# Kernel optimization log

Hardware: AMD Instinct MI355X
Metric: run time of the kernel (lower is better)

## Reference

```python
import jax, jax.numpy as jnp
import numpy as np

LN_EPS = 1e-5
BOUNDARY_ID = 0  # boundary_ids = {space_id} = {0}


def setup_inputs() -> dict:
    key = jax.random.key(0)
    k1, k2, k3 = jax.random.split(key, 3)
    B, T, D = 16, 8192, 256
    x = jax.random.normal(k1, (B, T, D), dtype=jnp.float32)
    input_ids = jax.random.randint(k2, (B, T), 0, 8, dtype=jnp.int64)
    W_proj = jax.random.normal(k3, (D, D), dtype=jnp.float32) / np.sqrt(D)
    b_proj = jnp.zeros((D,), dtype=jnp.float32)
    gamma = jnp.ones((D,), dtype=jnp.float32)
    beta = jnp.zeros((D,), dtype=jnp.float32)
    return {"x": x, "input_ids": input_ids, "W_proj": W_proj,
            "b_proj": b_proj, "gamma": gamma, "beta": beta}


def _pool(x, input_ids):
    # Boundary-defined segment mean pooling, vectorized via segment_sum.
    B, T, D = x.shape
    boundary = input_ids == BOUNDARY_ID                       # [B,T]
    nonb = ~boundary
    # A segment starts at a non-boundary token at t=0 or right after a boundary.
    prev_is_b = jnp.concatenate(
        [jnp.ones((B, 1), dtype=bool), boundary[:, :-1]], axis=1)
    start = nonb & prev_is_b
    seg = jnp.cumsum(start.astype(jnp.int32), axis=1) - 1     # seg idx per token
    MAXW = T  # static upper bound on number of segments (jit-safe padding)
    row_off = jnp.arange(B, dtype=jnp.int32)[:, None] * MAXW
    dump = B * MAXW  # boundary tokens go to a dummy segment, dropped below
    flat_ids = jnp.where(nonb, seg + row_off, dump).reshape(-1)
    sums = jax.ops.segment_sum(x.reshape(-1, D), flat_ids,
                               num_segments=B * MAXW + 1)[:-1]
    counts = jax.ops.segment_sum(jnp.ones((B * T,), x.dtype), flat_ids,
                                 num_segments=B * MAXW + 1)[:-1]
    sums = sums.reshape(B, MAXW, D)
    counts = counts.reshape(B, MAXW)
    mask = (counts > 0).astype(x.dtype)                       # [B,MAXW]
    padded = sums / jnp.maximum(counts, 1.0)[..., None]       # zeros where empty
    return padded, mask


def reference(x, input_ids, W_proj, b_proj, gamma, beta):
    padded, mask = _pool(x, input_ids)
    out = jnp.einsum('bwd,ed->bwe', padded, W_proj) + b_proj  # nn.Linear
    mu = jnp.mean(out, axis=-1, keepdims=True)
    var = jnp.mean(jnp.square(out - mu), axis=-1, keepdims=True)
    out = (out - mu) * jax.lax.rsqrt(var + LN_EPS) * gamma + beta
    return out, mask
```

## Files before the change

### kernel.cpp

```cpp
#include <hip/hip_runtime.h>
#include <hip/hip_bf16.h>
#include <math.h>

#define BB 16
#define TT 8192
#define DD 256
#define MAXSEG 4096
#define RPB 8
#define LN_EPS 1e-5f

typedef float vfloat4 __attribute__((ext_vector_type(4)));

__global__ __launch_bounds__(1024) void setup_kernel(
    const int* __restrict__ ids, const float* __restrict__ W,
    const float* __restrict__ bp, const float* __restrict__ gamma,
    const float* __restrict__ beta, int* __restrict__ counts,
    int* __restrict__ seg_start, int* __restrict__ nseg_g,
    float* __restrict__ mask_out, float* __restrict__ Wt,
    float* __restrict__ ln_empty) {
    __shared__ int wtot_s[16];
    __shared__ int wtot_n[16];
    __shared__ int segs[MAXSEG];
    __shared__ int pvals[MAXSEG];

    int tid = threadIdx.x;
    int lane = tid & 63;
    int wv = tid >> 6;

    if (blockIdx.x >= BB) {
        int bi = blockIdx.x - BB;
        if (bi < 64) {
            int d = bi * 4 + (tid >> 8);
            int e = tid & 255;
            Wt[d * DD + e] = W[e * DD + d];
        } else if (wv == 0) {
            int e0 = lane * 4;
            float4 v = *(const float4*)(bp + e0);
            float s = v.x + v.y + v.z + v.w;
            float sq = v.x * v.x + v.y * v.y + v.z * v.z + v.w * v.w;
#pragma unroll
            for (int o = 32; o > 0; o >>= 1) {
                s += __shfl_down(s, o);
                sq += __shfl_down(sq, o);
            }
            s = __shfl(s, 0);
            sq = __shfl(sq, 0);
            float mu = s * (1.f / (float)DD);
            float var = sq * (1.f / (float)DD) - mu * mu;
            float rs = rsqrtf(fmaxf(var, 0.f) + LN_EPS);
            float4 ge = *(const float4*)(gamma + e0);
            float4 be = *(const float4*)(beta + e0);
            float4 o4;
            o4.x = (v.x - mu) * rs * ge.x + be.x;
            o4.y = (v.y - mu) * rs * ge.y + be.y;
            o4.z = (v.z - mu) * rs * ge.z + be.z;
            o4.w = (v.w - mu) * rs * ge.w + be.w;
            *(float4*)(ln_empty + e0) = o4;
        }
        return;
    }

    const int TPT = 8;
    int b = blockIdx.x;
    const int* row = ids + b * TT;
    int t0 = tid * TPT;

    int4 q0 = ((const int4*)(row + t0))[0];
    int4 q1 = ((const int4*)(row + t0))[1];
    int v[TPT] = {q0.x, q0.y, q0.z, q0.w, q1.x, q1.y, q1.z, q1.w};
    int prev = (tid == 0) ? 0 : row[t0 - 1];

    bool nb[TPT], st[TPT];
    int cstart = 0, cnon = 0;
#pragma unroll
    for (int j = 0; j < TPT; ++j) {
        nb[j] = (v[j] != 0);
        int pv = (j == 0) ? prev : v[j - 1];
        st[j] = nb[j] && (pv == 0);
        cstart += st[j] ? 1 : 0;
        cnon += nb[j] ? 1 : 0;
    }

    int ss = cstart, sn = cnon;
#pragma unroll
    for (int o = 1; o < 64; o <<= 1) {
        int us = __shfl_up(ss, o);
        int un = __shfl_up(sn, o);
        if (lane >= o) { ss += us; sn += un; }
    }
    if (lane == 63) { wtot_s[wv] = ss; wtot_n[wv] = sn; }
    __syncthreads();

    int bs = 0, bn = 0, tot_s = 0, tot_n = 0;
#pragma unroll
    for (int j = 0; j < 16; ++j) {
        int a = wtot_s[j], c = wtot_n[j];
        if (j < wv) { bs += a; bn += c; }
        tot_s += a; tot_n += c;
    }
    bs += ss - cstart;
    bn += sn - cnon;

#pragma unroll
    for (int j = 0; j < TPT; ++j) {
        if (st[j]) { segs[bs] = t0 + j; pvals[bs] = bn; bs++; }
        bn += nb[j] ? 1 : 0;
    }
    __syncthreads();

    int ns = tot_s;
    for (int w = tid; w < TT; w += 1024) {
        int c = 0;
        if (w < ns) {
            int pe = (w + 1 < ns) ? pvals[w + 1] : tot_n;
            c = pe - pvals[w];
            seg_start[b * TT + w] = segs[w];
        }
        counts[b * TT + w] = c;
        mask_out[b * TT + w] = (w < ns) ? 1.0f : 0.0f;
    }
    if (tid == 0) nseg_g[b] = ns;
}

__global__ __launch_bounds__(256) void fused_kernel(
    const float* __restrict__ x, const float* __restrict__ Wt,
    const float* __restrict__ bp, const float* __restrict__ gamma,
    const float* __restrict__ beta, const int* __restrict__ counts,
    const int* __restrict__ seg_start, const int* __restrict__ nseg,
    const float* __restrict__ ln_e, float* __restrict__ out) {
    __shared__ float pooled[RPB][DD];
    __shared__ float red[4][RPB][2];

    int b = blockIdx.x;
    int wbase = blockIdx.y * RPB;
    int ns = nseg[b];
    int tid = threadIdx.x;
    int lane = tid & 63;
    int wv = tid >> 6;
    size_t rowbase = ((size_t)(b * TT + wbase)) * DD;

    if (wbase >= ns) {
        vfloat4 lv = *(const vfloat4*)(ln_e + 4 * lane);
        float* o = out + rowbase + 4 * lane;
#pragma unroll
        for (int rr = 0; rr < 2; ++rr) {
            int row = wv * 2 + rr;
            __builtin_nontemporal_store(lv, (vfloat4*)(o + (size_t)row * DD));
        }
        return;
    }
    int nr = min(RPB, ns - wbase);

#pragma unroll
    for (int rr = 0; rr < 2; ++rr) {
        int row = wv * 2 + rr;
        vfloat4 r = {0.f, 0.f, 0.f, 0.f};
        if (row < nr) {
            int w = wbase + row;
            int s = seg_start[b * TT + w];
            int len = counts[b * TT + w];
            const vfloat4* xp =
                (const vfloat4*)(x + ((size_t)(b * TT + s)) * DD) + lane;
            vfloat4 a[8];
#pragma unroll
            for (int j = 0; j < 8; ++j) a[j] = (vfloat4){0.f, 0.f, 0.f, 0.f};
            int t = 0;
            for (; t + 8 <= len; t += 8) {
#pragma unroll
                for (int j = 0; j < 8; ++j)
                    a[j] += __builtin_nontemporal_load(xp + (t + j) * 64);
            }
#pragma unroll
            for (int j = 0; j < 7; ++j)
                if (t + j < len)
                    a[j] += __builtin_nontemporal_load(xp + (t + j) * 64);
            r = ((a[0] + a[1]) + (a[2] + a[3])) + ((a[4] + a[5]) + (a[6] + a[7]));
            r *= (1.f / (float)len);
        }
        *(vfloat4*)&pooled[row][lane * 4] = r;
    }
    __syncthreads();

    int c = wv * 64 + lane;
    float acc[RPB];
    float bias = bp[c];
#pragma unroll
    for (int r = 0; r < RPB; ++r) acc[r] = bias;

    const float* Wc = Wt + c;
    float w0 = Wc[0 * DD];
    float w1 = Wc[1 * DD];
    float w2 = Wc[2 * DD];
    float w3 = Wc[3 * DD];
#pragma unroll 1
    for (int d0 = 0; d0 < DD; d0 += 4) {
        int dn = (d0 + 4) & 255;
        float n0 = Wc[(dn + 0) * DD];
        float n1 = Wc[(dn + 1) * DD];
        float n2 = Wc[(dn + 2) * DD];
        float n3 = Wc[(dn + 3) * DD];
#pragma unroll
        for (int r = 0; r < RPB; ++r) {
            const float4 p = *(const float4*)&pooled[r][d0];
            acc[r] = fmaf(p.x, w0, acc[r]);
            acc[r] = fmaf(p.y, w1, acc[r]);
            acc[r] = fmaf(p.z, w2, acc[r]);
            acc[r] = fmaf(p.w, w3, acc[r]);
        }
        w0 = n0; w1 = n1; w2 = n2; w3 = n3;
    }

#pragma unroll
    for (int r = 0; r < RPB; ++r) {
        float s = acc[r];
        float sq = acc[r] * acc[r];
#pragma unroll
        for (int o = 32; o > 0; o >>= 1) {
            s += __shfl_down(s, o);
            sq += __shfl_down(sq, o);
        }
        if (lane == 0) { red[wv][r][0] = s; red[wv][r][1] = sq; }
    }
    __syncthreads();

    float ga = gamma[c], be = beta[c];
#pragma unroll
    for (int r = 0; r < RPB; ++r) {
        float s = red[0][r][0] + red[1][r][0] + red[2][r][0] + red[3][r][0];
        float sq = red[0][r][1] + red[1][r][1] + red[2][r][1] + red[3][r][1];
        float mu = s * (1.f / (float)DD);
        float var = sq * (1.f / (float)DD) - mu * mu;
        float rs = rsqrtf(fmaxf(var, 0.f) + LN_EPS);
        float v = (acc[r] - mu) * rs * ga + be;
        __builtin_nontemporal_store(v, out + rowbase + (size_t)r * DD + c);
    }
}

extern "C" void kernel_launch(void* const* d_in, const int* in_sizes, int n_in,
                              void* d_out, int out_size, void* d_ws, size_t ws_size,
                              hipStream_t stream) {
    const float* x = (const float*)d_in[0];
    const int* ids = (const int*)d_in[1];
    const float* W = (const float*)d_in[2];
    const float* bp = (const float*)d_in[3];
    const float* gamma = (const float*)d_in[4];
    const float* beta = (const float*)d_in[5];

    float* out = (float*)d_out;
    float* mask = out + (size_t)BB * TT * DD;

    char* ws = (char*)d_ws;
    int* counts = (int*)ws;
    int* seg_start = (int*)(ws + (size_t)BB * TT * 4);
    int* nseg = (int*)(ws + (size_t)2 * BB * TT * 4);
    float* Wt = (float*)(ws + (size_t)2 * BB * TT * 4 + 256);
    float* ln_e = Wt + DD * DD;

    hipLaunchKernelGGL(setup_kernel, dim3(BB + 64 + 1), dim3(1024), 0, stream,
                       ids, W, bp, gamma, beta, counts, seg_start, nseg, mask,
                       Wt, ln_e);
    hipLaunchKernelGGL(fused_kernel, dim3(BB, TT / RPB), dim3(256), 0, stream,
                       x, Wt, bp, gamma, beta, counts, seg_start, nseg, ln_e, out);
}
```

Baseline: 270.9 us.

## Split fused pool+GEMM kernel into separate pooling and GEMM kernels

Moves segment mean pooling out of the fused kernel into a dedicated pool_kernel that writes pooled rows to a workspace buffer. The GEMM+LayerNorm kernel then reads pooled rows from global memory into registers, with a software prefetch of the next float4, instead of from shared memory. This gives the x-streaming phase its own launch shape and removes the pooling-then-GEMM barrier inside each block. The cost is an extra launch and a round trip of the pooled tensor through global memory. Pooled rows beyond MAXSEG per batch are assumed never to be needed.

```diff
diff --git a/kernel.cpp b/kernel.cpp
--- a/kernel.cpp
+++ b/kernel.cpp
@@ -122,13 +122,47 @@
     if (tid == 0) nseg_g[b] = ns;
 }
 
-__global__ __launch_bounds__(256) void fused_kernel(
-    const float* __restrict__ x, const float* __restrict__ Wt,
+__global__ __launch_bounds__(256) void pool_kernel(
+    const float* __restrict__ x, const int* __restrict__ counts,
+    const int* __restrict__ seg_start, const int* __restrict__ nseg,
+    float* __restrict__ pooled) {
+    int b = blockIdx.x;
+    int ns = nseg[b];
+    int ns8 = (ns + 7) & ~7;
+    int lane = threadIdx.x & 63;
+    int wv = threadIdx.x >> 6;
+    int w = blockIdx.y * 4 + wv;
+    if (w >= ns8) return;
+
+    vfloat4 r = {0.f, 0.f, 0.f, 0.f};
+    if (w < ns) {
+        int s = seg_start[b * TT + w];
+        int len = counts[b * TT + w];
+        const vfloat4* xp = (const vfloat4*)(x + ((size_t)(b * TT + s)) * DD) + lane;
+        vfloat4 a[8];
+#pragma unroll
+        for (int j = 0; j < 8; ++j) a[j] = (vfloat4){0.f, 0.f, 0.f, 0.f};
+        int t = 0;
+        for (; t + 8 <= len; t += 8) {
+#pragma unroll
+            for (int j = 0; j < 8; ++j)
+                a[j] += __builtin_nontemporal_load(xp + (t + j) * 64);
+        }
+#pragma unroll
+        for (int j = 0; j < 7; ++j)
+            if (t + j < len)
+                a[j] += __builtin_nontemporal_load(xp + (t + j) * 64);
+        r = ((a[0] + a[1]) + (a[2] + a[3])) + ((a[4] + a[5]) + (a[6] + a[7]));
+        r *= (1.f / (float)len);
+    }
+    *(vfloat4*)(pooled + ((size_t)(b * MAXSEG + w)) * DD + 4 * lane) = r;
+}
+
+__global__ __launch_bounds__(256) void gemm_fill(
+    const float* __restrict__ pooled, const float* __restrict__ Wt,
     const float* __restrict__ bp, const float* __restrict__ gamma,
-    const float* __restrict__ beta, const int* __restrict__ counts,
-    const int* __restrict__ seg_start, const int* __restrict__ nseg,
+    const float* __restrict__ beta, const int* __restrict__ nseg,
     const float* __restrict__ ln_e, float* __restrict__ out) {
-    __shared__ float pooled[RPB][DD];
     __shared__ float red[4][RPB][2];
 
     int b = blockIdx.x;
@@ -149,38 +183,8 @@
         }
         return;
     }
-    int nr = min(RPB, ns - wbase);
-
-#pragma unroll
-    for (int rr = 0; rr < 2; ++rr) {
-        int row = wv * 2 + rr;
-        vfloat4 r = {0.f, 0.f, 0.f, 0.f};
-        if (row < nr) {
-            int w = wbase + row;
-            int s = seg_start[b * TT + w];
-            int len = counts[b * TT + w];
-            const vfloat4* xp =
-                (const vfloat4*)(x + ((size_t)(b * TT + s)) * DD) + lane;
-            vfloat4 a[8];
-#pragma unroll
-            for (int j = 0; j < 8; ++j) a[j] = (vfloat4){0.f, 0.f, 0.f, 0.f};
-            int t = 0;
-            for (; t + 8 <= len; t += 8) {
-#pragma unroll
-                for (int j = 0; j < 8; ++j)
-                    a[j] += __builtin_nontemporal_load(xp + (t + j) * 64);
-            }
-#pragma unroll
-            for (int j = 0; j < 7; ++j)
-                if (t + j < len)
-                    a[j] += __builtin_nontemporal_load(xp + (t + j) * 64);
-            r = ((a[0] + a[1]) + (a[2] + a[3])) + ((a[4] + a[5]) + (a[6] + a[7]));
-            r *= (1.f / (float)len);
-        }
-        *(vfloat4*)&pooled[row][lane * 4] = r;
-    }
-    __syncthreads();
-
+
+    const float* P = pooled + ((size_t)(b * MAXSEG + wbase)) * DD;
     int c = wv * 64 + lane;
     float acc[RPB];
     float bias = bp[c];
@@ -192,6 +196,10 @@
     float w1 = Wc[1 * DD];
     float w2 = Wc[2 * DD];
     float w3 = Wc[3 * DD];
+    float4 p[RPB];
+#pragma unroll
+    for (int r = 0; r < RPB; ++r) p[r] = *(const float4*)(P + r * DD);
+
 #pragma unroll 1
     for (int d0 = 0; d0 < DD; d0 += 4) {
         int dn = (d0 + 4) & 255;
@@ -199,15 +207,19 @@
         float n1 = Wc[(dn + 1) * DD];
         float n2 = Wc[(dn + 2) * DD];
         float n3 = Wc[(dn + 3) * DD];
+        float4 np[RPB];
+#pragma unroll
+        for (int r = 0; r < RPB; ++r) np[r] = *(const float4*)(P + r * DD + dn);
 #pragma unroll
         for (int r = 0; r < RPB; ++r) {
-            const float4 p = *(const float4*)&pooled[r][d0];
-            acc[r] = fmaf(p.x, w0, acc[r]);
-            acc[r] = fmaf(p.y, w1, acc[r]);
-            acc[r] = fmaf(p.z, w2, acc[r]);
-            acc[r] = fmaf(p.w, w3, acc[r]);
+            acc[r] = fmaf(p[r].x, w0, acc[r]);
+            acc[r] = fmaf(p[r].y, w1, acc[r]);
+            acc[r] = fmaf(p[r].z, w2, acc[r]);
+            acc[r] = fmaf(p[r].w, w3, acc[r]);
         }
         w0 = n0; w1 = n1; w2 = n2; w3 = n3;
+#pragma unroll
+        for (int r = 0; r < RPB; ++r) p[r] = np[r];
     }
 
 #pragma unroll
@@ -255,10 +267,13 @@
     int* nseg = (int*)(ws + (size_t)2 * BB * TT * 4);
     float* Wt = (float*)(ws + (size_t)2 * BB * TT * 4 + 256);
     float* ln_e = Wt + DD * DD;
+    float* pooled = ln_e + DD;
 
     hipLaunchKernelGGL(setup_kernel, dim3(BB + 64 + 1), dim3(1024), 0, stream,
                        ids, W, bp, gamma, beta, counts, seg_start, nseg, mask,
                        Wt, ln_e);
-    hipLaunchKernelGGL(fused_kernel, dim3(BB, TT / RPB), dim3(256), 0, stream,
-                       x, Wt, bp, gamma, beta, counts, seg_start, nseg, ln_e, out);
-}
+    hipLaunchKernelGGL(pool_kernel, dim3(BB, MAXSEG / 4), dim3(256), 0, stream,
+                       x, counts, seg_start, nseg, pooled);
+    hipLaunchKernelGGL(gemm_fill, dim3(BB, TT / RPB), dim3(256), 0, stream,
+                       pooled, Wt, bp, gamma, beta, nseg, ln_e, out);
+}
```

Result: no change. 276.2 us (+1.9%).
